# Kernel tuning notes

Measured on AMD Instinct MI355X. Metric: run time of the kernel, lower is better.

Reference implementation:

```python
import jax, jax.numpy as jnp
import numpy as np

N = 50000      # neurons
R = 10         # max receptors per neuron
D = 5          # max delay (steps)
E = 10000000   # recurrent synapses
B = 1          # batch
DT = 1.0
LR_SCALE = 1.0
REC_DAMP = 0.4       # recurrent_dampening_factor
DAMPENING = 0.3      # dampening_factor (surrogate grad)


def setup_inputs() -> dict:
    key = jax.random.key(0)
    ks = jax.random.split(key, 20)
    inputs = jax.random.normal(ks[0], (B, R * N), jnp.float32) * 0.01
    z_buf = (jax.random.uniform(ks[1], (B, D * N)) < 0.02).astype(jnp.float32)
    v = jax.random.uniform(ks[2], (B, N), jnp.float32)
    r = jnp.zeros((B, N), jnp.float32)
    asc_1 = jax.random.normal(ks[3], (B, N), jnp.float32) * 0.01
    asc_2 = jax.random.normal(ks[4], (B, N), jnp.float32) * 0.01
    psc_rise = jax.random.uniform(ks[5], (B, R * N), jnp.float32) * 0.01
    psc = jax.random.uniform(ks[6], (B, R * N), jnp.float32) * 0.01
    rec_w = jax.random.normal(ks[7], (E,), jnp.float32) * 0.01
    rows = jax.random.randint(ks[8], (E,), 0, R * N, jnp.int32)
    cols = jax.random.randint(ks[9], (E,), 0, D * N, jnp.int32)
    rec_idx = jnp.stack([rows, cols], axis=1)
    # voltages are normalized by (V_th - E_L): v_th -> 1, e_l -> 0, v_reset -> 0
    v_th = jnp.ones((N,), jnp.float32)
    e_l = jnp.zeros((N,), jnp.float32)
    v_reset = jnp.zeros((N,), jnp.float32)
    g = jax.random.uniform(ks[10], (N,), jnp.float32, 3.0, 6.0)
    tau_m = jax.random.uniform(ks[11], (N,), jnp.float32, 5.0, 30.0)
    decay = jnp.exp(-DT / tau_m)
    current_factor = jax.random.uniform(ks[12], (N,), jnp.float32, 0.5, 1.5)
    t_ref = jnp.full((N,), 2.2, jnp.float32)
    k = jax.random.normal(ks[13], (N, 2), jnp.float32)  # stored in inv-sigmoid domain
    asc_amps = jax.random.normal(ks[14], (N, 2), jnp.float32) * 0.1
    tau_syn = jax.random.uniform(ks[15], (R * N,), jnp.float32, 2.0, 10.0)
    syn_decay = jnp.exp(-DT / tau_syn)
    psc_initial = jnp.asarray(np.e, jnp.float32) / tau_syn
    voltage_scale = jnp.full((N,), 30.0, jnp.float32)
    voltage_offset = jnp.full((N,), -70.0, jnp.float32)
    return dict(inputs=inputs, z_buf=z_buf, v=v, r=r, asc_1=asc_1, asc_2=asc_2,
                psc_rise=psc_rise, psc=psc, rec_w=rec_w, rec_idx=rec_idx,
                v_th=v_th, e_l=e_l, v_reset=v_reset, g=g, decay=decay,
                current_factor=current_factor, t_ref=t_ref, k=k, asc_amps=asc_amps,
                syn_decay=syn_decay, psc_initial=psc_initial,
                voltage_scale=voltage_scale, voltage_offset=voltage_offset)


def reference(inputs, z_buf, v, r, asc_1, asc_2, psc_rise, psc, rec_w, rec_idx,
              v_th, e_l, v_reset, g, decay, current_factor, t_ref, k, asc_amps,
              syn_decay, psc_initial, voltage_scale, voltage_offset):
    # one BillehColumn time step
    shaped = z_buf.reshape(B, D, N)          # (B, max_delay, N)
    prev_z = shaped[:, 0]
    # gradient-dampened spike buffer (fwd value identical to z_buf)
    dampened = z_buf * REC_DAMP
    rec_z = jax.lax.stop_gradient(z_buf - dampened) + dampened
    # sparse synaptic matmul: rows = neuron*R + receptor, cols = delay-slot neuron
    vals = rec_w[:, None] * rec_z.T[rec_idx[:, 1]]                       # (E, B)
    i_rec = jax.ops.segment_sum(vals, rec_idx[:, 0], num_segments=R * N).T  # (B, R*N)
    rec_inputs = i_rec * LR_SCALE + inputs
    # double-exponential synapse dynamics
    new_psc_rise = syn_decay * psc_rise + rec_inputs * psc_initial
    new_psc = psc * syn_decay + DT * syn_decay * psc_rise
    # refractory counter
    new_r = jnp.maximum(r + prev_z * t_ref - DT, 0.0)
    # after-spike currents (k stored in inv-sigmoid domain)
    kk = jax.nn.sigmoid(k)
    new_asc_1 = jnp.exp(-DT * kk[:, 0]) * asc_1 + prev_z * asc_amps[:, 0]
    new_asc_2 = jnp.exp(-DT * kk[:, 1]) * asc_2 + prev_z * asc_amps[:, 1]
    # membrane update: sum psc over receptors
    input_current = psc.reshape(B, N, R).sum(-1)
    new_v = decay * v + current_factor * (input_current + asc_1 + asc_2 + g * e_l)
    # surrogate-spike threshold (forward: heaviside)
    v_sc = (new_v - v_th) / (v_th - e_l)
    new_z = (v_sc > 0.0).astype(jnp.float32)
    new_z = jnp.where(new_r > 0.0, 0.0, new_z)
    # hard reset
    new_v = jnp.where(new_z > 0.5, jnp.broadcast_to(v_reset, new_v.shape), new_v)
    # shift delay buffer
    new_z_buf = jnp.concatenate([new_z[:, None], shaped[:, :-1]], axis=1).reshape(B, D * N)
    out_v = new_v * voltage_scale + voltage_offset
    return (new_z, out_v, new_z_buf, new_v, new_r, new_asc_1, new_asc_2,
            new_psc_rise, new_psc)
```

## Files before the change

### kernel.cpp

```cpp
#include <hip/hip_runtime.h>

namespace {

constexpr int N  = 50000;
constexpr int R  = 10;
constexpr int DD = 5;
constexpr int RN = R * N;
constexpr int DN = DD * N;
constexpr int E  = 10000000;
constexpr int EP = E / 2;
constexpr int EPH = EP / 2;

constexpr int ZB_BLOCKS = (DN + 255) / 256;
constexpr int ZB_WORDS  = ZB_BLOCKS * 256 / 32;

constexpr int AC_BLOCKS   = (RN / 4 + 255) / 256;
constexpr int NEUR_BLOCKS = (N + 255) / 256;
constexpr int PRE_BLOCKS  = ZB_BLOCKS + AC_BLOCKS + NEUR_BLOCKS;

constexpr int SC_BLOCK = 512;
constexpr int SC_GRID  = 1024;

constexpr int SYN_BLOCKS = (RN / 4 + 255) / 256;

__global__ __launch_bounds__(256) void pre_kernel(
    const float*  __restrict__ z_buf,
    unsigned int* __restrict__ bits,
    const float4* __restrict__ inputs,
    float4*       __restrict__ acc,
    const float*  __restrict__ v,
    const float*  __restrict__ r,
    const float*  __restrict__ asc1,
    const float*  __restrict__ asc2,
    const float*  __restrict__ psc,
    const float*  __restrict__ v_th,
    const float*  __restrict__ e_l,
    const float*  __restrict__ v_reset,
    const float*  __restrict__ g,
    const float*  __restrict__ decay,
    const float*  __restrict__ current_factor,
    const float*  __restrict__ t_ref,
    const float2* __restrict__ k,
    const float2* __restrict__ asc_amps,
    const float*  __restrict__ voltage_scale,
    const float*  __restrict__ voltage_offset,
    float*        __restrict__ out)
{
    int b = blockIdx.x;
    int tid = threadIdx.x;

    if (b < ZB_BLOCKS) {
        int i = b * 256 + tid;
        float zv = (i < DN) ? z_buf[i] : 0.0f;
        unsigned long long m = __ballot(zv != 0.0f);
        if ((tid & 63) == 0) {
            int w = i >> 5;
            bits[w]     = (unsigned int)m;
            bits[w + 1] = (unsigned int)(m >> 32);
        }
        return;
    }
    b -= ZB_BLOCKS;
    if (b < AC_BLOCKS) {
        int i = b * 256 + tid;
        if (i < RN / 4) acc[i] = inputs[i];
        return;
    }
    b -= AC_BLOCKS;
    {
        int n = b * 256 + tid;
        if (n >= N) return;

        float prev_z = z_buf[n];

        const float2* p2 = reinterpret_cast<const float2*>(psc + n * R);
        float ic = 0.0f;
#pragma unroll
        for (int t = 0; t < R / 2; ++t) {
            float2 pp = p2[t];
            ic += pp.x + pp.y;
        }

        float new_r = fmaxf(r[n] + prev_z * t_ref[n] - 1.0f, 0.0f);

        float2 kk = k[n];
        float2 aa = asc_amps[n];
        float s0 = 1.0f / (1.0f + expf(-kk.x));
        float s1 = 1.0f / (1.0f + expf(-kk.y));
        float a1_old = asc1[n];
        float a2_old = asc2[n];
        float new_a1 = expf(-s0) * a1_old + prev_z * aa.x;
        float new_a2 = expf(-s1) * a2_old + prev_z * aa.y;

        float el = e_l[n];
        float new_v = decay[n] * v[n]
                    + current_factor[n] * (ic + a1_old + a2_old + g[n] * el);

        float vth = v_th[n];
        float v_sc = (new_v - vth) / (vth - el);
        float nz = (v_sc > 0.0f) ? 1.0f : 0.0f;
        if (new_r > 0.0f) nz = 0.0f;
        if (nz > 0.5f) new_v = v_reset[n];

        out[0 * N + n]  = nz;
        out[1 * N + n]  = new_v * voltage_scale[n] + voltage_offset[n];
        out[2 * N + n]  = nz;
        out[7 * N + n]  = new_v;
        out[8 * N + n]  = new_r;
        out[9 * N + n]  = new_a1;
        out[10 * N + n] = new_a2;
    }
}

__device__ __forceinline__ void edge_pair(
    const int4 a, int p, const unsigned int* bits,
    const float* __restrict__ rec_w, float* __restrict__ acc)
{
    unsigned int w0 = bits[a.y >> 5];
    unsigned int w1 = bits[a.w >> 5];
    if ((w0 >> (a.y & 31)) & 1u) atomicAdd(acc + a.x, rec_w[2 * p]);
    if ((w1 >> (a.w & 31)) & 1u) atomicAdd(acc + a.z, rec_w[2 * p + 1]);
}

__global__ __launch_bounds__(SC_BLOCK) void scatter_kernel(
    const float* __restrict__ rec_w,
    const int4*  __restrict__ idx4,
    const unsigned int* __restrict__ bits_g,
    float*       __restrict__ acc,
    const float* __restrict__ z_buf,
    float*       __restrict__ out)
{
    __shared__ unsigned int bits[ZB_WORDS];
    {
        const uint4* src = reinterpret_cast<const uint4*>(bits_g);
        uint4* dst = reinterpret_cast<uint4*>(bits);
        for (int i = threadIdx.x; i < ZB_WORDS / 4; i += SC_BLOCK)
            dst[i] = src[i];
    }
    __syncthreads();

    const int gs  = SC_GRID * SC_BLOCK;
    const int gid = blockIdx.x * SC_BLOCK + threadIdx.x;

    int pA = gid, pB = gid + EPH;
    bool hA = pA < EPH;
    bool hB = pB < EP;
    int4 a = {0, 0, 0, 0}, b = {0, 0, 0, 0};
    if (hA) a = idx4[pA];
    if (hB) b = idx4[pB];
    while (hA || hB) {
        int nA = pA + gs, nB = pB + gs;
        bool hnA = hA && (nA < EPH);
        bool hnB = hB && (nB < EP);
        int4 na = {0, 0, 0, 0}, nb = {0, 0, 0, 0};
        if (hnA) na = idx4[nA];
        if (hnB) nb = idx4[nB];
        if (hA) edge_pair(a, pA, bits, rec_w, acc);
        if (hB) edge_pair(b, pB, bits, rec_w, acc);
        a = na; pA = nA; hA = hnA;
        b = nb; pB = nB; hB = hnB;
    }

    {
        const float4* src = reinterpret_cast<const float4*>(z_buf);
        float4* dst = reinterpret_cast<float4*>(out + 3 * N);
        for (int i = gid; i < (DN - N) / 4; i += gs)
            dst[i] = src[i];
    }
}

__global__ __launch_bounds__(256) void syn_kernel(
    const float4* __restrict__ acc,
    const float4* __restrict__ psc_rise,
    const float4* __restrict__ psc,
    const float4* __restrict__ syn_decay,
    const float4* __restrict__ psc_initial,
    float4* __restrict__ out_psc_rise,
    float4* __restrict__ out_psc,
    int n4)
{
    int j = blockIdx.x * 256 + threadIdx.x;
    if (j >= n4) return;
    float4 sd = syn_decay[j];
    float4 pr = psc_rise[j];
    float4 pi = psc_initial[j];
    float4 ac = acc[j];
    float4 ps = psc[j];
    float4 opr, ops;
    opr.x = sd.x * pr.x + ac.x * pi.x;
    opr.y = sd.y * pr.y + ac.y * pi.y;
    opr.z = sd.z * pr.z + ac.z * pi.z;
    opr.w = sd.w * pr.w + ac.w * pi.w;
    ops.x = ps.x * sd.x + sd.x * pr.x;
    ops.y = ps.y * sd.y + sd.y * pr.y;
    ops.z = ps.z * sd.z + sd.z * pr.z;
    ops.w = ps.w * sd.w + sd.w * pr.w;
    out_psc_rise[j] = opr;
    out_psc[j]      = ops;
}

}

extern "C" void kernel_launch(void* const* d_in, const int* in_sizes, int n_in,
                              void* d_out, int out_size, void* d_ws, size_t ws_size,
                              hipStream_t stream) {
    const float* inputs         = (const float*)d_in[0];
    const float* z_buf          = (const float*)d_in[1];
    const float* v              = (const float*)d_in[2];
    const float* r              = (const float*)d_in[3];
    const float* asc1           = (const float*)d_in[4];
    const float* asc2           = (const float*)d_in[5];
    const float* psc_rise       = (const float*)d_in[6];
    const float* psc            = (const float*)d_in[7];
    const float* rec_w          = (const float*)d_in[8];
    const int*   rec_idx        = (const int*)d_in[9];
    const float* v_th           = (const float*)d_in[10];
    const float* e_l            = (const float*)d_in[11];
    const float* v_reset        = (const float*)d_in[12];
    const float* g              = (const float*)d_in[13];
    const float* decay          = (const float*)d_in[14];
    const float* current_factor = (const float*)d_in[15];
    const float* t_ref          = (const float*)d_in[16];
    const float* k              = (const float*)d_in[17];
    const float* asc_amps       = (const float*)d_in[18];
    const float* syn_decay      = (const float*)d_in[19];
    const float* psc_initial    = (const float*)d_in[20];
    const float* voltage_scale  = (const float*)d_in[21];
    const float* voltage_offset = (const float*)d_in[22];

    float* out = (float*)d_out;
    float* acc = (float*)d_ws;
    unsigned int* bits = (unsigned int*)(acc + RN);

    pre_kernel<<<PRE_BLOCKS, 256, 0, stream>>>(
        z_buf, bits, (const float4*)inputs, (float4*)acc,
        v, r, asc1, asc2, psc, v_th, e_l, v_reset, g, decay,
        current_factor, t_ref, (const float2*)k, (const float2*)asc_amps,
        voltage_scale, voltage_offset, out);

    scatter_kernel<<<SC_GRID, SC_BLOCK, 0, stream>>>(
        rec_w, (const int4*)rec_idx, bits, acc, z_buf, out);

    syn_kernel<<<SYN_BLOCKS, 256, 0, stream>>>(
        (const float4*)acc, (const float4*)psc_rise, (const float4*)psc,
        (const float4*)syn_decay, (const float4*)psc_initial,
        (float4*)(out + 11 * N), (float4*)(out + 21 * N), RN / 4);
}
```

Baseline: 34.88 us.

## Fold synaptic update into pre-kernel and scatter scaled weights into output

The synaptic-current update now runs inside the pre-kernel, seeding the psc_rise output with the decayed value plus inputs times psc_initial. The scatter kernel then atomically adds rec_w times psc_initial straight into that output, so the accumulator workspace and the third kernel launch are gone. This saves a launch and a full 500K-element read and write pass. In exchange, each active edge makes an extra gather of psc_initial, and the summation order changes slightly, which can alter floating-point rounding.

```diff
diff --git a/kernel.cpp b/kernel.cpp
--- a/kernel.cpp
+++ b/kernel.cpp
@@ -14,25 +14,25 @@
 constexpr int ZB_BLOCKS = (DN + 255) / 256;
 constexpr int ZB_WORDS  = ZB_BLOCKS * 256 / 32;
 
-constexpr int AC_BLOCKS   = (RN / 4 + 255) / 256;
+constexpr int SEED_BLOCKS = (RN / 4 + 255) / 256;
 constexpr int NEUR_BLOCKS = (N + 255) / 256;
-constexpr int PRE_BLOCKS  = ZB_BLOCKS + AC_BLOCKS + NEUR_BLOCKS;
+constexpr int PRE_BLOCKS  = ZB_BLOCKS + SEED_BLOCKS + NEUR_BLOCKS;
 
 constexpr int SC_BLOCK = 512;
 constexpr int SC_GRID  = 1024;
-
-constexpr int SYN_BLOCKS = (RN / 4 + 255) / 256;
 
 __global__ __launch_bounds__(256) void pre_kernel(
     const float*  __restrict__ z_buf,
     unsigned int* __restrict__ bits,
-    const float4* __restrict__ inputs,
-    float4*       __restrict__ acc,
+    const float4* __restrict__ inputs4,
+    const float*  __restrict__ psc_rise,
+    const float*  __restrict__ psc,
+    const float*  __restrict__ syn_decay,
+    const float*  __restrict__ psc_initial,
     const float*  __restrict__ v,
     const float*  __restrict__ r,
     const float*  __restrict__ asc1,
     const float*  __restrict__ asc2,
-    const float*  __restrict__ psc,
     const float*  __restrict__ v_th,
     const float*  __restrict__ e_l,
     const float*  __restrict__ v_reset,
@@ -61,12 +61,34 @@
         return;
     }
     b -= ZB_BLOCKS;
-    if (b < AC_BLOCKS) {
-        int i = b * 256 + tid;
-        if (i < RN / 4) acc[i] = inputs[i];
+    if (b < SEED_BLOCKS) {
+        int j = b * 256 + tid;
+        if (j >= RN / 4) return;
+        const float4* pr4 = reinterpret_cast<const float4*>(psc_rise);
+        const float4* ps4 = reinterpret_cast<const float4*>(psc);
+        const float4* sd4 = reinterpret_cast<const float4*>(syn_decay);
+        const float4* pi4 = reinterpret_cast<const float4*>(psc_initial);
+        float4* opr4 = reinterpret_cast<float4*>(out + 11 * N);
+        float4* ops4 = reinterpret_cast<float4*>(out + 21 * N);
+        float4 sd = sd4[j];
+        float4 pr = pr4[j];
+        float4 pi = pi4[j];
+        float4 in = inputs4[j];
+        float4 ps = ps4[j];
+        float4 opr, ops;
+        opr.x = sd.x * pr.x + in.x * pi.x;
+        opr.y = sd.y * pr.y + in.y * pi.y;
+        opr.z = sd.z * pr.z + in.z * pi.z;
+        opr.w = sd.w * pr.w + in.w * pi.w;
+        ops.x = ps.x * sd.x + sd.x * pr.x;
+        ops.y = ps.y * sd.y + sd.y * pr.y;
+        ops.z = ps.z * sd.z + sd.z * pr.z;
+        ops.w = ps.w * sd.w + sd.w * pr.w;
+        opr4[j] = opr;
+        ops4[j] = ops;
         return;
     }
-    b -= AC_BLOCKS;
+    b -= SEED_BLOCKS;
     {
         int n = b * 256 + tid;
         if (n >= N) return;
@@ -114,19 +136,22 @@
 
 __device__ __forceinline__ void edge_pair(
     const int4 a, int p, const unsigned int* bits,
-    const float* __restrict__ rec_w, float* __restrict__ acc)
+    const float* __restrict__ rec_w, const float* __restrict__ pinit,
+    float* __restrict__ opr)
 {
     unsigned int w0 = bits[a.y >> 5];
     unsigned int w1 = bits[a.w >> 5];
-    if ((w0 >> (a.y & 31)) & 1u) atomicAdd(acc + a.x, rec_w[2 * p]);
-    if ((w1 >> (a.w & 31)) & 1u) atomicAdd(acc + a.z, rec_w[2 * p + 1]);
+    if ((w0 >> (a.y & 31)) & 1u)
+        atomicAdd(opr + a.x, rec_w[2 * p] * pinit[a.x]);
+    if ((w1 >> (a.w & 31)) & 1u)
+        atomicAdd(opr + a.z, rec_w[2 * p + 1] * pinit[a.z]);
 }
 
 __global__ __launch_bounds__(SC_BLOCK) void scatter_kernel(
     const float* __restrict__ rec_w,
     const int4*  __restrict__ idx4,
     const unsigned int* __restrict__ bits_g,
-    float*       __restrict__ acc,
+    const float* __restrict__ pinit,
     const float* __restrict__ z_buf,
     float*       __restrict__ out)
 {
@@ -138,6 +163,8 @@
             dst[i] = src[i];
     }
     __syncthreads();
+
+    float* opr = out + 11 * N;
 
     const int gs  = SC_GRID * SC_BLOCK;
     const int gid = blockIdx.x * SC_BLOCK + threadIdx.x;
@@ -155,8 +182,8 @@
         int4 na = {0, 0, 0, 0}, nb = {0, 0, 0, 0};
         if (hnA) na = idx4[nA];
         if (hnB) nb = idx4[nB];
-        if (hA) edge_pair(a, pA, bits, rec_w, acc);
-        if (hB) edge_pair(b, pB, bits, rec_w, acc);
+        if (hA) edge_pair(a, pA, bits, rec_w, pinit, opr);
+        if (hB) edge_pair(b, pB, bits, rec_w, pinit, opr);
         a = na; pA = nA; hA = hnA;
         b = nb; pB = nB; hB = hnB;
     }
@@ -167,36 +194,6 @@
         for (int i = gid; i < (DN - N) / 4; i += gs)
             dst[i] = src[i];
     }
-}
-
-__global__ __launch_bounds__(256) void syn_kernel(
-    const float4* __restrict__ acc,
-    const float4* __restrict__ psc_rise,
-    const float4* __restrict__ psc,
-    const float4* __restrict__ syn_decay,
-    const float4* __restrict__ psc_initial,
-    float4* __restrict__ out_psc_rise,
-    float4* __restrict__ out_psc,
-    int n4)
-{
-    int j = blockIdx.x * 256 + threadIdx.x;
-    if (j >= n4) return;
-    float4 sd = syn_decay[j];
-    float4 pr = psc_rise[j];
-    float4 pi = psc_initial[j];
-    float4 ac = acc[j];
-    float4 ps = psc[j];
-    float4 opr, ops;
-    opr.x = sd.x * pr.x + ac.x * pi.x;
-    opr.y = sd.y * pr.y + ac.y * pi.y;
-    opr.z = sd.z * pr.z + ac.z * pi.z;
-    opr.w = sd.w * pr.w + ac.w * pi.w;
-    ops.x = ps.x * sd.x + sd.x * pr.x;
-    ops.y = ps.y * sd.y + sd.y * pr.y;
-    ops.z = ps.z * sd.z + sd.z * pr.z;
-    ops.w = ps.w * sd.w + sd.w * pr.w;
-    out_psc_rise[j] = opr;
-    out_psc[j]      = ops;
 }
 
 }
@@ -229,20 +226,14 @@
     const float* voltage_offset = (const float*)d_in[22];
 
     float* out = (float*)d_out;
-    float* acc = (float*)d_ws;
-    unsigned int* bits = (unsigned int*)(acc + RN);
+    unsigned int* bits = (unsigned int*)d_ws;
 
     pre_kernel<<<PRE_BLOCKS, 256, 0, stream>>>(
-        z_buf, bits, (const float4*)inputs, (float4*)acc,
-        v, r, asc1, asc2, psc, v_th, e_l, v_reset, g, decay,
+        z_buf, bits, (const float4*)inputs, psc_rise, psc, syn_decay,
+        psc_initial, v, r, asc1, asc2, v_th, e_l, v_reset, g, decay,
         current_factor, t_ref, (const float2*)k, (const float2*)asc_amps,
         voltage_scale, voltage_offset, out);
 
     scatter_kernel<<<SC_GRID, SC_BLOCK, 0, stream>>>(
-        rec_w, (const int4*)rec_idx, bits, acc, z_buf, out);
-
-    syn_kernel<<<SYN_BLOCKS, 256, 0, stream>>>(
-        (const float4*)acc, (const float4*)psc_rise, (const float4*)psc,
-        (const float4*)syn_decay, (const float4*)psc_initial,
-        (float4*)(out + 11 * N), (float4*)(out + 21 * N), RN / 4);
-}
+        rec_w, (const int4*)rec_idx, bits, psc_initial, z_buf, out);
+}
```

After: 33.12 us. 1.05x faster.
